# Kernel tuning notes

Measured on AMD Instinct MI355X. Metric: run time of the kernel, lower is better.

Reference implementation:

```python
import jax, jax.numpy as jnp
import numpy as np

E = 32      # num_experts
K = 4       # num_experts_per_tok
C = 1280


def setup_inputs() -> dict:
    key = jax.random.key(0)
    k0, k1, k2, k3, k4 = jax.random.split(key, 5)
    B, S, D, I = 4, 2048, 1024, 512
    return {
        "hidden_states": jax.random.normal(k0, (B, S, D), jnp.float32),
        "router_w": jax.random.normal(k1, (E, D), jnp.float32) * 0.02,   # nn.Linear(hidden, E).weight
        "gate_w": jax.random.normal(k2, (E, I, D), jnp.float32) * 0.02,
        "up_w": jax.random.normal(k3, (E, I, D), jnp.float32) * 0.02,
        "down_w": jax.random.normal(k4, (E, D, I), jnp.float32) * 0.02,
    }


def reference(hidden_states, router_w, gate_w, up_w, down_w):
    B, S, D = hidden_states.shape
    x = hidden_states.reshape(-1, D)                       # [T, D]
    T = x.shape[0]

    # Router: softmax in fp32, top-k, renormalize (norm_topk_prob=True)
    router_logits = x @ router_w.T                          # [T, E]
    probs = jax.nn.softmax(router_logits.astype(jnp.float32), axis=-1)
    w, sel = jax.lax.top_k(probs, K)                        # [T, K]
    w = w / jnp.sum(w, axis=-1, keepdims=True)
    w = w.astype(x.dtype)

    # Flatten (token, slot) dispatch rows
    e_flat = sel.reshape(-1)                                # [T*K]
    tok = jnp.repeat(jnp.arange(T), K)                      # [T*K]

    # Position of each row within its expert's buffer
    oh = jax.nn.one_hot(e_flat, E, dtype=jnp.int32)         # [T*K, E]
    pos = jnp.take_along_axis(jnp.cumsum(oh, axis=0), e_flat[:, None], axis=1)[:, 0] - 1
    valid = pos < C

    # Dispatch: scatter tokens into [E, C, D]; overflow rows go to slot C and are dropped
    pos_w = jnp.minimum(pos, C)
    buf = jnp.zeros((E, C + 1, D), x.dtype).at[e_flat, pos_w].set(x[tok])[:, :C]

    # Per-expert SwiGLU MLP as grouped matmuls
    g = jnp.einsum('ecd,eid->eci', buf, gate_w)
    u = jnp.einsum('ecd,eid->eci', buf, up_w)
    h = jax.nn.silu(g) * u
    y = jnp.einsum('eci,edi->ecd', h, down_w)               # [E, C, D]

    # Combine: gather expert outputs back and scatter-add into tokens
    pos_r = jnp.minimum(pos, C - 1)
    gathered = y[e_flat, pos_r]                             # [T*K, D]
    coef = w.reshape(-1) * valid.astype(x.dtype)
    final = jax.ops.segment_sum(gathered * coef[:, None], tok, num_segments=T)

    return final.reshape(B, S, D), router_logits
```

## Files before the change

### kernel.cpp

```cpp
#include <hip/hip_runtime.h>

#define T_TOK 8192
#define D_DIM 1024
#define E_NUM 32
#define K_TOP 4
#define CAP 1280
#define I_DIM 512

typedef float f32x4 __attribute__((ext_vector_type(4)));
typedef short s16x8 __attribute__((ext_vector_type(8)));

static __device__ __forceinline__ unsigned short f2bf(float f) {
    unsigned int u = __float_as_uint(f);
    unsigned int r = (u + 0x7fffu + ((u >> 16) & 1u)) >> 16;
    return (unsigned short)r;
}
static __device__ __forceinline__ float bf2f(unsigned short s) {
    return __uint_as_float(((unsigned int)s) << 16);
}

static __device__ __forceinline__ void gload16(const unsigned short* g, unsigned short* l) {
    __builtin_amdgcn_global_load_lds(
        (const __attribute__((address_space(1))) unsigned int*)g,
        (__attribute__((address_space(3))) unsigned int*)l,
        16, 0, 0);
}

#define GW_F4 4194304L
__global__ __launch_bounds__(256) void cvt_kernel(
    const float* __restrict__ gw,
    const float* __restrict__ uw, const float* __restrict__ dw,
    unsigned short* __restrict__ gbf,
    unsigned short* __restrict__ ubf, unsigned short* __restrict__ dbf) {
    long i = (long)blockIdx.x * 256 + threadIdx.x;
    const float* src; unsigned short* dst; long off;
    if (i < GW_F4)        { src = gw; dst = gbf; off = i; }
    else if (i < 2*GW_F4) { src = uw; dst = ubf; off = i - GW_F4; }
    else                  { src = dw; dst = dbf; off = i - 2*GW_F4; }
    float4 v = ((const float4*)src)[off];
    ushort4 b;
    b.x = f2bf(v.x); b.y = f2bf(v.y); b.z = f2bf(v.z); b.w = f2bf(v.w);
    ((ushort4*)dst)[off] = b;
}

__global__ __launch_bounds__(256) void router_kernel(
    const float* __restrict__ x, const float* __restrict__ rw,
    float* __restrict__ logits, unsigned short* __restrict__ xbf) {
    int t = (blockIdx.x * 256 + threadIdx.x) >> 6;
    int lane = threadIdx.x & 63;
    const float* xr = x + (size_t)t * D_DIM;
    float xf[16];
#pragma unroll
    for (int j = 0; j < 16; ++j) xf[j] = xr[lane + 64 * j];
    unsigned short* xb = xbf + (size_t)t * D_DIM;
#pragma unroll
    for (int j = 0; j < 16; ++j) xb[lane + 64 * j] = f2bf(xf[j]);
#pragma unroll 1
    for (int e = 0; e < E_NUM; ++e) {
        const float* wr = rw + (size_t)e * D_DIM;
        float acc = 0.f;
#pragma unroll
        for (int j = 0; j < 16; ++j) acc = fmaf(xf[j], wr[lane + 64 * j], acc);
#pragma unroll
        for (int off = 32; off; off >>= 1) acc += __shfl_xor(acc, off);
        if (lane == 0) logits[(size_t)t * E_NUM + e] = acc;
    }
}

__global__ __launch_bounds__(256) void topk_kernel(
    const float* __restrict__ logits,
    int* __restrict__ counts, int* __restrict__ rowtok,
    int* __restrict__ tokslot, float* __restrict__ tokcoef) {
    __shared__ float lg[256 * 33];
    __shared__ int hist[E_NUM];
    __shared__ int base[E_NUM];
    int tid = threadIdx.x;
    int t0 = blockIdx.x * 256;
    if (tid < E_NUM) hist[tid] = 0;
#pragma unroll
    for (int i = 0; i < E_NUM; ++i) {
        int idx = i * 256 + tid;
        lg[(idx >> 5) * 33 + (idx & 31)] = logits[(size_t)t0 * E_NUM + idx];
    }
    __syncthreads();

    float p[E_NUM];
    float m = -1e30f;
#pragma unroll
    for (int e = 0; e < E_NUM; ++e) { p[e] = lg[tid * 33 + e]; m = fmaxf(m, p[e]); }
#pragma unroll
    for (int e = 0; e < E_NUM; ++e) p[e] = __expf(p[e] - m);

    float wv[K_TOP]; int sel[K_TOP];
#pragma unroll
    for (int k = 0; k < K_TOP; ++k) {
        float best = -1.0f; int bi = 0;
#pragma unroll
        for (int e = 0; e < E_NUM; ++e) if (p[e] > best) { best = p[e]; bi = e; }
        wv[k] = best; sel[k] = bi; p[bi] = -2.0f;
    }

    int lofs[K_TOP];
#pragma unroll
    for (int k = 0; k < K_TOP; ++k) lofs[k] = atomicAdd(&hist[sel[k]], 1);
    __syncthreads();
    if (tid < E_NUM) base[tid] = atomicAdd(&counts[tid], hist[tid]);
    __syncthreads();

    float inv = 1.0f / (wv[0] + wv[1] + wv[2] + wv[3]);
    int t = t0 + tid;
#pragma unroll
    for (int k = 0; k < K_TOP; ++k) {
        int e = sel[k];
        int slot = base[e] + lofs[k];
        if (slot < CAP) {
            rowtok[e * CAP + slot] = t;
            tokslot[t * K_TOP + k] = e * CAP + slot;
        } else {
            tokslot[t * K_TOP + k] = -1;
        }
        tokcoef[t * K_TOP + k] = wv[k] * inv;
    }
}

__global__ __launch_bounds__(512, 2) void gateup_kernel(
    const unsigned short* __restrict__ xbf,
    const unsigned short* __restrict__ gbf, const unsigned short* __restrict__ ubf,
    const int* __restrict__ counts, const int* __restrict__ rowtok,
    unsigned short* __restrict__ h_ws) {
    int bid = blockIdx.x;
    int xcd = bid & 7;
    int slot = bid >> 3;
    int e = xcd + 8 * (slot / 20);
    int r = slot % 20;
    int mt = r >> 2;
    int nt = r & 3;
    int n_e = counts[e]; if (n_e > CAP) n_e = CAP;
    if (mt * 256 >= n_e) return;

    __shared__ unsigned short As[2][256 * 64];
    __shared__ unsigned short Bg[2][128 * 64];
    __shared__ unsigned short Bu[2][128 * 64];
    __shared__ int toks[256];

    int tid = threadIdx.x, lane = tid & 63, wv = tid >> 6;
    if (tid < 256) {
        int rr = mt * 256 + tid;
        toks[tid] = (rr < n_e) ? rowtok[e * CAP + rr] : rowtok[e * CAP];
    }
    __syncthreads();

    int row8 = tid >> 3;
    int c8 = (((tid & 7) ^ (row8 & 7)) * 8);
    int ldst = tid * 8;
    const unsigned short* aB[4];
#pragma unroll
    for (int j = 0; j < 4; ++j)
        aB[j] = xbf + (size_t)toks[j * 64 + row8] * D_DIM + c8;
    const unsigned short* gB[2];
    const unsigned short* uB[2];
#pragma unroll
    for (int j = 0; j < 2; ++j) {
        gB[j] = gbf + ((size_t)e * I_DIM + nt * 128 + j * 64 + row8) * D_DIM + c8;
        uB[j] = ubf + ((size_t)e * I_DIM + nt * 128 + j * 64 + row8) * D_DIM + c8;
    }

    int wm = (wv >> 1) * 64;
    int wn = (wv & 1) * 64;
    int fr = lane & 15;
    int fc = (lane >> 4) * 8;
    int fsw = (fr & 7) << 3;

    f32x4 accg[4][4] = {};
    f32x4 accu[4][4] = {};

    auto stage = [&](int kt) {
        int q = kt & 1, k2 = kt * 64;
#pragma unroll
        for (int j = 0; j < 4; ++j) gload16(aB[j] + k2, &As[q][j * 4096 + ldst]);
#pragma unroll
        for (int j = 0; j < 2; ++j) {
            gload16(gB[j] + k2, &Bg[q][j * 4096 + ldst]);
            gload16(uB[j] + k2, &Bu[q][j * 4096 + ldst]);
        }
    };
    auto compute = [&](int p) {
#pragma unroll
        for (int kk = 0; kk < 2; ++kk) {
            s16x8 af[4], bgf[4], buf_[4];
#pragma unroll
            for (int mi = 0; mi < 4; ++mi)
                af[mi] = *(const s16x8*)&As[p][(wm + mi * 16 + fr) * 64 + ((kk * 32 + fc) ^ fsw)];
#pragma unroll
            for (int ni = 0; ni < 4; ++ni) {
                bgf[ni]  = *(const s16x8*)&Bg[p][(wn + ni * 16 + fr) * 64 + ((kk * 32 + fc) ^ fsw)];
                buf_[ni] = *(const s16x8*)&Bu[p][(wn + ni * 16 + fr) * 64 + ((kk * 32 + fc) ^ fsw)];
            }
#pragma unroll
            for (int mi = 0; mi < 4; ++mi)
#pragma unroll
                for (int ni = 0; ni < 4; ++ni) {
                    accg[mi][ni] = __builtin_amdgcn_mfma_f32_16x16x32_bf16(af[mi], bgf[ni],  accg[mi][ni], 0, 0, 0);
                    accu[mi][ni] = __builtin_amdgcn_mfma_f32_16x16x32_bf16(af[mi], buf_[ni], accu[mi][ni], 0, 0, 0);
                }
        }
    };

    stage(0); stage(1);
    for (int kt = 0; kt < 15; ++kt) {
        int p = kt & 1;
        asm volatile("s_waitcnt vmcnt(8)" ::: "memory");
        asm volatile("s_barrier" ::: "memory");
        __builtin_amdgcn_s_setprio(1);
        compute(p);
        __builtin_amdgcn_s_setprio(0);
        asm volatile("s_barrier" ::: "memory");
        if (kt < 14) stage(kt + 2);
    }
    asm volatile("s_waitcnt vmcnt(0)" ::: "memory");
    asm volatile("s_barrier" ::: "memory");
    __builtin_amdgcn_s_setprio(1);
    compute(1);
    __builtin_amdgcn_s_setprio(0);

    int rq = (lane >> 4) * 4;
    int cq = lane & 15;
#pragma unroll
    for (int mi = 0; mi < 4; ++mi)
#pragma unroll
        for (int ni = 0; ni < 4; ++ni)
#pragma unroll
            for (int rr = 0; rr < 4; ++rr) {
                int grow = mt * 256 + wm + mi * 16 + rq + rr;
                if (grow < n_e) {
                    float g = accg[mi][ni][rr];
                    float hv = g / (1.0f + __expf(-g)) * accu[mi][ni][rr];
                    int icol = nt * 128 + wn + ni * 16 + cq;
                    h_ws[((size_t)e * CAP + grow) * I_DIM + icol] = f2bf(hv);
                }
            }
}

__global__ __launch_bounds__(512, 2) void down_kernel(
    const unsigned short* __restrict__ h_ws, const unsigned short* __restrict__ dbf,
    const int* __restrict__ counts, unsigned short* __restrict__ y_ws) {
    int bid = blockIdx.x;
    int xcd = bid & 7;
    int slot = bid >> 3;
    int e = xcd + 8 * (slot / 20);
    int r = slot % 20;
    int mt = r >> 2;
    int nt = r & 3;
    int n_e = counts[e]; if (n_e > CAP) n_e = CAP;
    if (mt * 256 >= n_e) return;

    __shared__ unsigned short As[2][256 * 64];
    __shared__ unsigned short Bd[2][256 * 64];

    int tid = threadIdx.x, lane = tid & 63, wv = tid >> 6;

    int row8 = tid >> 3;
    int c8 = (((tid & 7) ^ (row8 & 7)) * 8);
    int ldst = tid * 8;
    const unsigned short* aB[4];
    const unsigned short* bB[4];
#pragma unroll
    for (int j = 0; j < 4; ++j) {
        aB[j] = h_ws + ((size_t)e * CAP + mt * 256 + j * 64 + row8) * I_DIM + c8;
        bB[j] = dbf  + ((size_t)e * D_DIM + nt * 256 + j * 64 + row8) * I_DIM + c8;
    }

    int wm = (wv >> 2) * 128;
    int wn = (wv & 3) * 64;
    int fr = lane & 15;
    int fc = (lane >> 4) * 8;
    int fsw = (fr & 7) << 3;

    f32x4 acc[8][4] = {};

    auto stage = [&](int kt) {
        int q = kt & 1, k2 = kt * 64;
#pragma unroll
        for (int j = 0; j < 4; ++j) {
            gload16(aB[j] + k2, &As[q][j * 4096 + ldst]);
            gload16(bB[j] + k2, &Bd[q][j * 4096 + ldst]);
        }
    };
    auto compute = [&](int p) {
#pragma unroll
        for (int kk = 0; kk < 2; ++kk) {
            s16x8 af[8], bf[4];
#pragma unroll
            for (int mi = 0; mi < 8; ++mi)
                af[mi] = *(const s16x8*)&As[p][(wm + mi * 16 + fr) * 64 + ((kk * 32 + fc) ^ fsw)];
#pragma unroll
            for (int ni = 0; ni < 4; ++ni)
                bf[ni] = *(const s16x8*)&Bd[p][(wn + ni * 16 + fr) * 64 + ((kk * 32 + fc) ^ fsw)];
#pragma unroll
            for (int mi = 0; mi < 8; ++mi)
#pragma unroll
                for (int ni = 0; ni < 4; ++ni)
                    acc[mi][ni] = __builtin_amdgcn_mfma_f32_16x16x32_bf16(af[mi], bf[ni], acc[mi][ni], 0, 0, 0);
        }
    };

    stage(0); stage(1);
    for (int kt = 0; kt < 7; ++kt) {
        int p = kt & 1;
        asm volatile("s_waitcnt vmcnt(8)" ::: "memory");
        asm volatile("s_barrier" ::: "memory");
        __builtin_amdgcn_s_setprio(1);
        compute(p);
        __builtin_amdgcn_s_setprio(0);
        asm volatile("s_barrier" ::: "memory");
        if (kt < 6) stage(kt + 2);
    }
    asm volatile("s_waitcnt vmcnt(0)" ::: "memory");
    asm volatile("s_barrier" ::: "memory");
    __builtin_amdgcn_s_setprio(1);
    compute(1);
    __builtin_amdgcn_s_setprio(0);

    int rq = (lane >> 4) * 4;
    int cq = lane & 15;
#pragma unroll
    for (int mi = 0; mi < 8; ++mi)
#pragma unroll
        for (int ni = 0; ni < 4; ++ni)
#pragma unroll
            for (int rr = 0; rr < 4; ++rr) {
                int grow = mt * 256 + wm + mi * 16 + rq + rr;
                if (grow < n_e) {
                    int dcol = nt * 256 + wn + ni * 16 + cq;
                    y_ws[((size_t)e * CAP + grow) * D_DIM + dcol] = f2bf(acc[mi][ni][rr]);
                }
            }
}

__global__ __launch_bounds__(256) void combine_kernel(
    const unsigned short* __restrict__ y_ws,
    const int* __restrict__ tokslot, const float* __restrict__ tokcoef,
    float* __restrict__ out) {
    int t = (blockIdx.x * 256 + threadIdx.x) >> 6;
    int lane = threadIdx.x & 63;
    float acc[16] = {};
#pragma unroll
    for (int k = 0; k < K_TOP; ++k) {
        int slot = tokslot[t * K_TOP + k];
        if (slot >= 0) {
            float c = tokcoef[t * K_TOP + k];
            const unsigned short* row = y_ws + (size_t)slot * D_DIM + lane * 16;
            s16x8 v0 = *(const s16x8*)row;
            s16x8 v1 = *(const s16x8*)(row + 8);
#pragma unroll
            for (int j = 0; j < 8; ++j) acc[j]     = fmaf(c, bf2f((unsigned short)v0[j]), acc[j]);
#pragma unroll
            for (int j = 0; j < 8; ++j) acc[8 + j] = fmaf(c, bf2f((unsigned short)v1[j]), acc[8 + j]);
        }
    }
    float* o = out + (size_t)t * D_DIM + lane * 16;
#pragma unroll
    for (int j = 0; j < 4; ++j)
        ((float4*)o)[j] = make_float4(acc[4 * j], acc[4 * j + 1], acc[4 * j + 2], acc[4 * j + 3]);
}

extern "C" void kernel_launch(void* const* d_in, const int* in_sizes, int n_in,
                              void* d_out, int out_size, void* d_ws, size_t ws_size,
                              hipStream_t stream) {
    const float* x  = (const float*)d_in[0];
    const float* rw = (const float*)d_in[1];
    const float* gw = (const float*)d_in[2];
    const float* uw = (const float*)d_in[3];
    const float* dw = (const float*)d_in[4];
    float* out = (float*)d_out;
    float* logits = out + (size_t)T_TOK * D_DIM;

    char* ws = (char*)d_ws;
    size_t off = 0;
    unsigned short* xbf = (unsigned short*)(ws + off); off += (size_t)T_TOK * D_DIM * 2;
    unsigned short* gbf = (unsigned short*)(ws + off); off += (size_t)E_NUM * I_DIM * D_DIM * 2;
    unsigned short* ubf = (unsigned short*)(ws + off); off += (size_t)E_NUM * I_DIM * D_DIM * 2;
    unsigned short* y_ws = xbf;
    unsigned short* dbf = (unsigned short*)(ws + off); off += (size_t)E_NUM * D_DIM * I_DIM * 2;
    unsigned short* h_ws = (unsigned short*)(ws + off); off += (size_t)E_NUM * CAP * I_DIM * 2;
    int* counts = (int*)(ws + off); off += 256;
    int* rowtok = (int*)(ws + off); off += (size_t)E_NUM * CAP * 4;
    int* tokslot = (int*)(ws + off); off += (size_t)T_TOK * K_TOP * 4;
    float* tokcoef = (float*)(ws + off); off += (size_t)T_TOK * K_TOP * 4;

    hipMemsetAsync(counts, 0, E_NUM * 4, stream);

    cvt_kernel<<<(int)((3 * GW_F4) / 256), 256, 0, stream>>>(gw, uw, dw, gbf, ubf, dbf);
    router_kernel<<<T_TOK / 4, 256, 0, stream>>>(x, rw, logits, xbf);
    topk_kernel<<<T_TOK / 256, 256, 0, stream>>>(logits, counts, rowtok, tokslot, tokcoef);
    gateup_kernel<<<E_NUM * (CAP / 256) * (I_DIM / 128), 512, 0, stream>>>(xbf, gbf, ubf, counts, rowtok, h_ws);
    down_kernel<<<E_NUM * (CAP / 256) * (D_DIM / 256), 512, 0, stream>>>(h_ws, dbf, counts, y_ws);
    combine_kernel<<<T_TOK / 4, 256, 0, stream>>>(y_ws, tokslot, tokcoef, out);
}
```

Measured before the change: 465.1 us.

## Use 4-stage BK=32 LDS pipeline with single barrier per step in MoE GEMMs

Both the gate/up and down grouped GEMMs switch from a double-buffered 64-wide K tile to a four-deep ring of 32-wide K tiles. Each step issues the next loads right after one barrier, which drops the second barrier per iteration. It also changes the LDS swizzle for the narrower rows. The aim is to keep three tiles of loads in flight and cut synchronisation stalls. In exchange there are twice as many loop iterations and barriers per unit of K, and a new XOR pattern that may bring back bank conflicts.

```diff
diff --git a/kernel.cpp b/kernel.cpp
--- a/kernel.cpp
+++ b/kernel.cpp
@@ -138,9 +138,9 @@
     int n_e = counts[e]; if (n_e > CAP) n_e = CAP;
     if (mt * 256 >= n_e) return;
 
-    __shared__ unsigned short As[2][256 * 64];
-    __shared__ unsigned short Bg[2][128 * 64];
-    __shared__ unsigned short Bu[2][128 * 64];
+    __shared__ unsigned short As[4][256 * 32];
+    __shared__ unsigned short Bg[4][128 * 32];
+    __shared__ unsigned short Bu[4][128 * 32];
     __shared__ int toks[256];
 
     int tid = threadIdx.x, lane = tid & 63, wv = tid >> 6;
@@ -150,78 +150,58 @@
     }
     __syncthreads();
 
-    int row8 = tid >> 3;
-    int c8 = (((tid & 7) ^ (row8 & 7)) * 8);
+    int rA0 = tid >> 2;
+    int csw = ((tid & 3) ^ ((tid >> 3) & 3)) * 8;
+    const unsigned short* gaA0 = xbf + (size_t)toks[rA0] * D_DIM + csw;
+    const unsigned short* gaA1 = xbf + (size_t)toks[128 + rA0] * D_DIM + csw;
+    const unsigned short* gaG  = gbf + ((size_t)e * I_DIM + nt * 128 + rA0) * D_DIM + csw;
+    const unsigned short* gaU  = ubf + ((size_t)e * I_DIM + nt * 128 + rA0) * D_DIM + csw;
     int ldst = tid * 8;
-    const unsigned short* aB[4];
-#pragma unroll
-    for (int j = 0; j < 4; ++j)
-        aB[j] = xbf + (size_t)toks[j * 64 + row8] * D_DIM + c8;
-    const unsigned short* gB[2];
-    const unsigned short* uB[2];
-#pragma unroll
-    for (int j = 0; j < 2; ++j) {
-        gB[j] = gbf + ((size_t)e * I_DIM + nt * 128 + j * 64 + row8) * D_DIM + c8;
-        uB[j] = ubf + ((size_t)e * I_DIM + nt * 128 + j * 64 + row8) * D_DIM + c8;
-    }
 
     int wm = (wv >> 1) * 64;
     int wn = (wv & 1) * 64;
     int fr = lane & 15;
-    int fc = (lane >> 4) * 8;
-    int fsw = (fr & 7) << 3;
+    int pcol = (((lane >> 4) ^ ((fr >> 1) & 3)) * 8);
 
     f32x4 accg[4][4] = {};
     f32x4 accu[4][4] = {};
 
     auto stage = [&](int kt) {
-        int q = kt & 1, k2 = kt * 64;
-#pragma unroll
-        for (int j = 0; j < 4; ++j) gload16(aB[j] + k2, &As[q][j * 4096 + ldst]);
-#pragma unroll
-        for (int j = 0; j < 2; ++j) {
-            gload16(gB[j] + k2, &Bg[q][j * 4096 + ldst]);
-            gload16(uB[j] + k2, &Bu[q][j * 4096 + ldst]);
+        int b = kt & 3, k2 = kt * 32;
+        gload16(gaA0 + k2, &As[b][ldst]);
+        gload16(gaA1 + k2, &As[b][4096 + ldst]);
+        gload16(gaG  + k2, &Bg[b][ldst]);
+        gload16(gaU  + k2, &Bu[b][ldst]);
+    };
+
+    stage(0); stage(1); stage(2);
+    for (int kt = 0; kt < 32; ++kt) {
+        int b = kt & 3;
+        if (kt < 30)       asm volatile("s_waitcnt vmcnt(8)" ::: "memory");
+        else if (kt == 30) asm volatile("s_waitcnt vmcnt(4)" ::: "memory");
+        else               asm volatile("s_waitcnt vmcnt(0)" ::: "memory");
+        asm volatile("s_barrier" ::: "memory");
+        if (kt + 3 < 32) stage(kt + 3);
+
+        s16x8 af[4], bgf[4], buf_[4];
+#pragma unroll
+        for (int mi = 0; mi < 4; ++mi)
+            af[mi] = *(const s16x8*)&As[b][(wm + mi * 16 + fr) * 32 + pcol];
+#pragma unroll
+        for (int ni = 0; ni < 4; ++ni) {
+            bgf[ni]  = *(const s16x8*)&Bg[b][(wn + ni * 16 + fr) * 32 + pcol];
+            buf_[ni] = *(const s16x8*)&Bu[b][(wn + ni * 16 + fr) * 32 + pcol];
         }
-    };
-    auto compute = [&](int p) {
-#pragma unroll
-        for (int kk = 0; kk < 2; ++kk) {
-            s16x8 af[4], bgf[4], buf_[4];
-#pragma unroll
-            for (int mi = 0; mi < 4; ++mi)
-                af[mi] = *(const s16x8*)&As[p][(wm + mi * 16 + fr) * 64 + ((kk * 32 + fc) ^ fsw)];
+        __builtin_amdgcn_s_setprio(1);
+#pragma unroll
+        for (int mi = 0; mi < 4; ++mi)
 #pragma unroll
             for (int ni = 0; ni < 4; ++ni) {
-                bgf[ni]  = *(const s16x8*)&Bg[p][(wn + ni * 16 + fr) * 64 + ((kk * 32 + fc) ^ fsw)];
-                buf_[ni] = *(const s16x8*)&Bu[p][(wn + ni * 16 + fr) * 64 + ((kk * 32 + fc) ^ fsw)];
+                accg[mi][ni] = __builtin_amdgcn_mfma_f32_16x16x32_bf16(af[mi], bgf[ni],  accg[mi][ni], 0, 0, 0);
+                accu[mi][ni] = __builtin_amdgcn_mfma_f32_16x16x32_bf16(af[mi], buf_[ni], accu[mi][ni], 0, 0, 0);
             }
-#pragma unroll
-            for (int mi = 0; mi < 4; ++mi)
-#pragma unroll
-                for (int ni = 0; ni < 4; ++ni) {
-                    accg[mi][ni] = __builtin_amdgcn_mfma_f32_16x16x32_bf16(af[mi], bgf[ni],  accg[mi][ni], 0, 0, 0);
-                    accu[mi][ni] = __builtin_amdgcn_mfma_f32_16x16x32_bf16(af[mi], buf_[ni], accu[mi][ni], 0, 0, 0);
-                }
-        }
-    };
-
-    stage(0); stage(1);
-    for (int kt = 0; kt < 15; ++kt) {
-        int p = kt & 1;
-        asm volatile("s_waitcnt vmcnt(8)" ::: "memory");
-        asm volatile("s_barrier" ::: "memory");
-        __builtin_amdgcn_s_setprio(1);
-        compute(p);
         __builtin_amdgcn_s_setprio(0);
-        asm volatile("s_barrier" ::: "memory");
-        if (kt < 14) stage(kt + 2);
-    }
-    asm volatile("s_waitcnt vmcnt(0)" ::: "memory");
-    asm volatile("s_barrier" ::: "memory");
-    __builtin_amdgcn_s_setprio(1);
-    compute(1);
-    __builtin_amdgcn_s_setprio(0);
+    }
 
     int rq = (lane >> 4) * 4;
     int cq = lane & 15;
@@ -254,72 +234,58 @@
     int n_e = counts[e]; if (n_e > CAP) n_e = CAP;
     if (mt * 256 >= n_e) return;
 
-    __shared__ unsigned short As[2][256 * 64];
-    __shared__ unsigned short Bd[2][256 * 64];
+    __shared__ unsigned short As[4][256 * 32];
+    __shared__ unsigned short Bd[4][256 * 32];
 
     int tid = threadIdx.x, lane = tid & 63, wv = tid >> 6;
 
-    int row8 = tid >> 3;
-    int c8 = (((tid & 7) ^ (row8 & 7)) * 8);
+    int rA0 = tid >> 2;
+    int csw = ((tid & 3) ^ ((tid >> 3) & 3)) * 8;
+    const unsigned short* gaA0 = h_ws + ((size_t)e * CAP + mt * 256 + rA0) * I_DIM + csw;
+    const unsigned short* gaA1 = h_ws + ((size_t)e * CAP + mt * 256 + 128 + rA0) * I_DIM + csw;
+    const unsigned short* gaB0 = dbf  + ((size_t)e * D_DIM + nt * 256 + rA0) * I_DIM + csw;
+    const unsigned short* gaB1 = dbf  + ((size_t)e * D_DIM + nt * 256 + 128 + rA0) * I_DIM + csw;
     int ldst = tid * 8;
-    const unsigned short* aB[4];
-    const unsigned short* bB[4];
-#pragma unroll
-    for (int j = 0; j < 4; ++j) {
-        aB[j] = h_ws + ((size_t)e * CAP + mt * 256 + j * 64 + row8) * I_DIM + c8;
-        bB[j] = dbf  + ((size_t)e * D_DIM + nt * 256 + j * 64 + row8) * I_DIM + c8;
-    }
 
     int wm = (wv >> 2) * 128;
     int wn = (wv & 3) * 64;
     int fr = lane & 15;
-    int fc = (lane >> 4) * 8;
-    int fsw = (fr & 7) << 3;
+    int pcol = (((lane >> 4) ^ ((fr >> 1) & 3)) * 8);
 
     f32x4 acc[8][4] = {};
 
     auto stage = [&](int kt) {
-        int q = kt & 1, k2 = kt * 64;
-#pragma unroll
-        for (int j = 0; j < 4; ++j) {
-            gload16(aB[j] + k2, &As[q][j * 4096 + ldst]);
-            gload16(bB[j] + k2, &Bd[q][j * 4096 + ldst]);
-        }
+        int b = kt & 3, k2 = kt * 32;
+        gload16(gaA0 + k2, &As[b][ldst]);
+        gload16(gaA1 + k2, &As[b][4096 + ldst]);
+        gload16(gaB0 + k2, &Bd[b][ldst]);
+        gload16(gaB1 + k2, &Bd[b][4096 + ldst]);
     };
-    auto compute = [&](int p) {
-#pragma unroll
-        for (int kk = 0; kk < 2; ++kk) {
-            s16x8 af[8], bf[4];
-#pragma unroll
-            for (int mi = 0; mi < 8; ++mi)
-                af[mi] = *(const s16x8*)&As[p][(wm + mi * 16 + fr) * 64 + ((kk * 32 + fc) ^ fsw)];
+
+    stage(0); stage(1); stage(2);
+    for (int kt = 0; kt < 16; ++kt) {
+        int b = kt & 3;
+        if (kt < 14)       asm volatile("s_waitcnt vmcnt(8)" ::: "memory");
+        else if (kt == 14) asm volatile("s_waitcnt vmcnt(4)" ::: "memory");
+        else               asm volatile("s_waitcnt vmcnt(0)" ::: "memory");
+        asm volatile("s_barrier" ::: "memory");
+        if (kt + 3 < 16) stage(kt + 3);
+
+        s16x8 af[8], bf[4];
+#pragma unroll
+        for (int mi = 0; mi < 8; ++mi)
+            af[mi] = *(const s16x8*)&As[b][(wm + mi * 16 + fr) * 32 + pcol];
+#pragma unroll
+        for (int ni = 0; ni < 4; ++ni)
+            bf[ni] = *(const s16x8*)&Bd[b][(wn + ni * 16 + fr) * 32 + pcol];
+        __builtin_amdgcn_s_setprio(1);
+#pragma unroll
+        for (int mi = 0; mi < 8; ++mi)
 #pragma unroll
             for (int ni = 0; ni < 4; ++ni)
-                bf[ni] = *(const s16x8*)&Bd[p][(wn + ni * 16 + fr) * 64 + ((kk * 32 + fc) ^ fsw)];
-#pragma unroll
-            for (int mi = 0; mi < 8; ++mi)
-#pragma unroll
-                for (int ni = 0; ni < 4; ++ni)
-                    acc[mi][ni] = __builtin_amdgcn_mfma_f32_16x16x32_bf16(af[mi], bf[ni], acc[mi][ni], 0, 0, 0);
-        }
-    };
-
-    stage(0); stage(1);
-    for (int kt = 0; kt < 7; ++kt) {
-        int p = kt & 1;
-        asm volatile("s_waitcnt vmcnt(8)" ::: "memory");
-        asm volatile("s_barrier" ::: "memory");
-        __builtin_amdgcn_s_setprio(1);
-        compute(p);
+                acc[mi][ni] = __builtin_amdgcn_mfma_f32_16x16x32_bf16(af[mi], bf[ni], acc[mi][ni], 0, 0, 0);
         __builtin_amdgcn_s_setprio(0);
-        asm volatile("s_barrier" ::: "memory");
-        if (kt < 6) stage(kt + 2);
-    }
-    asm volatile("s_waitcnt vmcnt(0)" ::: "memory");
-    asm volatile("s_barrier" ::: "memory");
-    __builtin_amdgcn_s_setprio(1);
-    compute(1);
-    __builtin_amdgcn_s_setprio(0);
+    }
 
     int rq = (lane >> 4) * 4;
     int cq = lane & 15;
```

Measured after the change: 495.1 us. 6.5% more time.

## Make gate-up and down GEMMs loop over m-tiles with fixed grid

Applied to the files above, without the earlier changes.

Launches a fixed grid of 8 blocks per expert for both expert GEMM kernels; each block handles one n-tile and iterates over alternating m-tiles of its expert instead of one block per (m,n) tile. This is meant to remove the launch overhead of early-exit blocks for empty tiles and reuse weight tiles across m iterations. It risks lower occupancy (one block per CU) and serialized tiles lengthening the critical path.

```diff
diff --git a/kernel.cpp b/kernel.cpp
--- a/kernel.cpp
+++ b/kernel.cpp
@@ -129,14 +129,11 @@
     const int* __restrict__ counts, const int* __restrict__ rowtok,
     unsigned short* __restrict__ h_ws) {
     int bid = blockIdx.x;
-    int xcd = bid & 7;
-    int slot = bid >> 3;
-    int e = xcd + 8 * (slot / 20);
-    int r = slot % 20;
-    int mt = r >> 2;
-    int nt = r & 3;
+    int e = (bid & 7) + 8 * (bid >> 6);
+    int rem = (bid >> 3) & 7;
+    int nt = rem >> 1;
+    int h = rem & 1;
     int n_e = counts[e]; if (n_e > CAP) n_e = CAP;
-    if (mt * 256 >= n_e) return;
 
     __shared__ unsigned short As[2][256 * 64];
     __shared__ unsigned short Bg[2][128 * 64];
@@ -144,19 +141,10 @@
     __shared__ int toks[256];
 
     int tid = threadIdx.x, lane = tid & 63, wv = tid >> 6;
-    if (tid < 256) {
-        int rr = mt * 256 + tid;
-        toks[tid] = (rr < n_e) ? rowtok[e * CAP + rr] : rowtok[e * CAP];
-    }
-    __syncthreads();
 
     int row8 = tid >> 3;
     int c8 = (((tid & 7) ^ (row8 & 7)) * 8);
     int ldst = tid * 8;
-    const unsigned short* aB[4];
-#pragma unroll
-    for (int j = 0; j < 4; ++j)
-        aB[j] = xbf + (size_t)toks[j * 64 + row8] * D_DIM + c8;
     const unsigned short* gB[2];
     const unsigned short* uB[2];
 #pragma unroll
@@ -170,89 +158,100 @@
     int fr = lane & 15;
     int fc = (lane >> 4) * 8;
     int fsw = (fr & 7) << 3;
-
-    f32x4 accg[4][4] = {};
-    f32x4 accu[4][4] = {};
-
-    auto stage = [&](int kt) {
-        int q = kt & 1, k2 = kt * 64;
-#pragma unroll
-        for (int j = 0; j < 4; ++j) gload16(aB[j] + k2, &As[q][j * 4096 + ldst]);
-#pragma unroll
-        for (int j = 0; j < 2; ++j) {
-            gload16(gB[j] + k2, &Bg[q][j * 4096 + ldst]);
-            gload16(uB[j] + k2, &Bu[q][j * 4096 + ldst]);
+    int rq = (lane >> 4) * 4;
+    int cq = lane & 15;
+
+    for (int mt = h; mt < 5 && mt * 256 < n_e; mt += 2) {
+        __syncthreads();
+        if (tid < 256) {
+            int rr = mt * 256 + tid;
+            toks[tid] = (rr < n_e) ? rowtok[e * CAP + rr] : rowtok[e * CAP];
         }
-    };
-    auto compute = [&](int p) {
-#pragma unroll
-        for (int kk = 0; kk < 2; ++kk) {
-            s16x8 af[4], bgf[4], buf_[4];
-#pragma unroll
-            for (int mi = 0; mi < 4; ++mi)
-                af[mi] = *(const s16x8*)&As[p][(wm + mi * 16 + fr) * 64 + ((kk * 32 + fc) ^ fsw)];
-#pragma unroll
-            for (int ni = 0; ni < 4; ++ni) {
-                bgf[ni]  = *(const s16x8*)&Bg[p][(wn + ni * 16 + fr) * 64 + ((kk * 32 + fc) ^ fsw)];
-                buf_[ni] = *(const s16x8*)&Bu[p][(wn + ni * 16 + fr) * 64 + ((kk * 32 + fc) ^ fsw)];
+        __syncthreads();
+
+        const unsigned short* aB[4];
+#pragma unroll
+        for (int j = 0; j < 4; ++j)
+            aB[j] = xbf + (size_t)toks[j * 64 + row8] * D_DIM + c8;
+
+        f32x4 accg[4][4] = {};
+        f32x4 accu[4][4] = {};
+
+        auto stage = [&](int kt) {
+            int q = kt & 1, k2 = kt * 64;
+#pragma unroll
+            for (int j = 0; j < 4; ++j) gload16(aB[j] + k2, &As[q][j * 4096 + ldst]);
+#pragma unroll
+            for (int j = 0; j < 2; ++j) {
+                gload16(gB[j] + k2, &Bg[q][j * 4096 + ldst]);
+                gload16(uB[j] + k2, &Bu[q][j * 4096 + ldst]);
             }
-#pragma unroll
-            for (int mi = 0; mi < 4; ++mi)
+        };
+        auto compute = [&](int p) {
+#pragma unroll
+            for (int kk = 0; kk < 2; ++kk) {
+                s16x8 af[4], bgf[4], buf_[4];
+#pragma unroll
+                for (int mi = 0; mi < 4; ++mi)
+                    af[mi] = *(const s16x8*)&As[p][(wm + mi * 16 + fr) * 64 + ((kk * 32 + fc) ^ fsw)];
 #pragma unroll
                 for (int ni = 0; ni < 4; ++ni) {
-                    accg[mi][ni] = __builtin_amdgcn_mfma_f32_16x16x32_bf16(af[mi], bgf[ni],  accg[mi][ni], 0, 0, 0);
-                    accu[mi][ni] = __builtin_amdgcn_mfma_f32_16x16x32_bf16(af[mi], buf_[ni], accu[mi][ni], 0, 0, 0);
+                    bgf[ni]  = *(const s16x8*)&Bg[p][(wn + ni * 16 + fr) * 64 + ((kk * 32 + fc) ^ fsw)];
+                    buf_[ni] = *(const s16x8*)&Bu[p][(wn + ni * 16 + fr) * 64 + ((kk * 32 + fc) ^ fsw)];
                 }
+#pragma unroll
+                for (int mi = 0; mi < 4; ++mi)
+#pragma unroll
+                    for (int ni = 0; ni < 4; ++ni) {
+                        accg[mi][ni] = __builtin_amdgcn_mfma_f32_16x16x32_bf16(af[mi], bgf[ni],  accg[mi][ni], 0, 0, 0);
+                        accu[mi][ni] = __builtin_amdgcn_mfma_f32_16x16x32_bf16(af[mi], buf_[ni], accu[mi][ni], 0, 0, 0);
+                    }
+            }
+        };
+
+        stage(0); stage(1);
+        for (int kt = 0; kt < 15; ++kt) {
+            int p = kt & 1;
+            asm volatile("s_waitcnt vmcnt(8)" ::: "memory");
+            asm volatile("s_barrier" ::: "memory");
+            __builtin_amdgcn_s_setprio(1);
+            compute(p);
+            __builtin_amdgcn_s_setprio(0);
+            asm volatile("s_barrier" ::: "memory");
+            if (kt < 14) stage(kt + 2);
         }
-    };
-
-    stage(0); stage(1);
-    for (int kt = 0; kt < 15; ++kt) {
-        int p = kt & 1;
-        asm volatile("s_waitcnt vmcnt(8)" ::: "memory");
+        asm volatile("s_waitcnt vmcnt(0)" ::: "memory");
         asm volatile("s_barrier" ::: "memory");
         __builtin_amdgcn_s_setprio(1);
-        compute(p);
+        compute(1);
         __builtin_amdgcn_s_setprio(0);
-        asm volatile("s_barrier" ::: "memory");
-        if (kt < 14) stage(kt + 2);
-    }
-    asm volatile("s_waitcnt vmcnt(0)" ::: "memory");
-    asm volatile("s_barrier" ::: "memory");
-    __builtin_amdgcn_s_setprio(1);
-    compute(1);
-    __builtin_amdgcn_s_setprio(0);
-
-    int rq = (lane >> 4) * 4;
-    int cq = lane & 15;
-#pragma unroll
-    for (int mi = 0; mi < 4; ++mi)
-#pragma unroll
-        for (int ni = 0; ni < 4; ++ni)
-#pragma unroll
-            for (int rr = 0; rr < 4; ++rr) {
-                int grow = mt * 256 + wm + mi * 16 + rq + rr;
-                if (grow < n_e) {
-                    float g = accg[mi][ni][rr];
-                    float hv = g / (1.0f + __expf(-g)) * accu[mi][ni][rr];
-                    int icol = nt * 128 + wn + ni * 16 + cq;
-                    h_ws[((size_t)e * CAP + grow) * I_DIM + icol] = f2bf(hv);
+
+#pragma unroll
+        for (int mi = 0; mi < 4; ++mi)
+#pragma unroll
+            for (int ni = 0; ni < 4; ++ni)
+#pragma unroll
+                for (int rr = 0; rr < 4; ++rr) {
+                    int grow = mt * 256 + wm + mi * 16 + rq + rr;
+                    if (grow < n_e) {
+                        float g = accg[mi][ni][rr];
+                        float hv = g / (1.0f + __expf(-g)) * accu[mi][ni][rr];
+                        int icol = nt * 128 + wn + ni * 16 + cq;
+                        h_ws[((size_t)e * CAP + grow) * I_DIM + icol] = f2bf(hv);
+                    }
                 }
-            }
+    }
 }
 
 __global__ __launch_bounds__(512, 2) void down_kernel(
     const unsigned short* __restrict__ h_ws, const unsigned short* __restrict__ dbf,
     const int* __restrict__ counts, unsigned short* __restrict__ y_ws) {
     int bid = blockIdx.x;
-    int xcd = bid & 7;
-    int slot = bid >> 3;
-    int e = xcd + 8 * (slot / 20);
-    int r = slot % 20;
-    int mt = r >> 2;
-    int nt = r & 3;
+    int e = (bid & 7) + 8 * (bid >> 6);
+    int rem = (bid >> 3) & 7;
+    int nt = rem >> 1;
+    int h = rem & 1;
     int n_e = counts[e]; if (n_e > CAP) n_e = CAP;
-    if (mt * 256 >= n_e) return;
 
     __shared__ unsigned short As[2][256 * 64];
     __shared__ unsigned short Bd[2][256 * 64];
@@ -262,79 +261,85 @@
     int row8 = tid >> 3;
     int c8 = (((tid & 7) ^ (row8 & 7)) * 8);
     int ldst = tid * 8;
-    const unsigned short* aB[4];
     const unsigned short* bB[4];
 #pragma unroll
-    for (int j = 0; j < 4; ++j) {
-        aB[j] = h_ws + ((size_t)e * CAP + mt * 256 + j * 64 + row8) * I_DIM + c8;
-        bB[j] = dbf  + ((size_t)e * D_DIM + nt * 256 + j * 64 + row8) * I_DIM + c8;
-    }
+    for (int j = 0; j < 4; ++j)
+        bB[j] = dbf + ((size_t)e * D_DIM + nt * 256 + j * 64 + row8) * I_DIM + c8;
 
     int wm = (wv >> 2) * 128;
     int wn = (wv & 3) * 64;
     int fr = lane & 15;
     int fc = (lane >> 4) * 8;
     int fsw = (fr & 7) << 3;
-
-    f32x4 acc[8][4] = {};
-
-    auto stage = [&](int kt) {
-        int q = kt & 1, k2 = kt * 64;
-#pragma unroll
-        for (int j = 0; j < 4; ++j) {
-            gload16(aB[j] + k2, &As[q][j * 4096 + ldst]);
-            gload16(bB[j] + k2, &Bd[q][j * 4096 + ldst]);
+    int rq = (lane >> 4) * 4;
+    int cq = lane & 15;
+
+    for (int mt = h; mt < 5 && mt * 256 < n_e; mt += 2) {
+        __syncthreads();
+
+        const unsigned short* aB[4];
+#pragma unroll
+        for (int j = 0; j < 4; ++j)
+            aB[j] = h_ws + ((size_t)e * CAP + mt * 256 + j * 64 + row8) * I_DIM + c8;
+
+        f32x4 acc[8][4] = {};
+
+        auto stage = [&](int kt) {
+            int q = kt & 1, k2 = kt * 64;
+#pragma unroll
+            for (int j = 0; j < 4; ++j) {
+                gload16(aB[j] + k2, &As[q][j * 4096 + ldst]);
+                gload16(bB[j] + k2, &Bd[q][j * 4096 + ldst]);
+            }
+        };
+        auto compute = [&](int p) {
+#pragma unroll
+            for (int kk = 0; kk < 2; ++kk) {
+                s16x8 af[8], bf[4];
+#pragma unroll
+                for (int mi = 0; mi < 8; ++mi)
+                    af[mi] = *(const s16x8*)&As[p][(wm + mi * 16 + fr) * 64 + ((kk * 32 + fc) ^ fsw)];
+#pragma unroll
+                for (int ni = 0; ni < 4; ++ni)
+                    bf[ni] = *(const s16x8*)&Bd[p][(wn + ni * 16 + fr) * 64 + ((kk * 32 + fc) ^ fsw)];
+#pragma unroll
+                for (int mi = 0; mi < 8; ++mi)
+#pragma unroll
+                    for (int ni = 0; ni < 4; ++ni)
+                        acc[mi][ni] = __builtin_amdgcn_mfma_f32_16x16x32_bf16(af[mi], bf[ni], acc[mi][ni], 0, 0, 0);
+            }
+        };
+
+        stage(0); stage(1);
+        for (int kt = 0; kt < 7; ++kt) {
+            int p = kt & 1;
+            asm volatile("s_waitcnt vmcnt(8)" ::: "memory");
+            asm volatile("s_barrier" ::: "memory");
+            __builtin_amdgcn_s_setprio(1);
+            compute(p);
+            __builtin_amdgcn_s_setprio(0);
+            asm volatile("s_barrier" ::: "memory");
+            if (kt < 6) stage(kt + 2);
         }
-    };
-    auto compute = [&](int p) {
-#pragma unroll
-        for (int kk = 0; kk < 2; ++kk) {
-            s16x8 af[8], bf[4];
-#pragma unroll
-            for (int mi = 0; mi < 8; ++mi)
-                af[mi] = *(const s16x8*)&As[p][(wm + mi * 16 + fr) * 64 + ((kk * 32 + fc) ^ fsw)];
-#pragma unroll
-            for (int ni = 0; ni < 4; ++ni)
-                bf[ni] = *(const s16x8*)&Bd[p][(wn + ni * 16 + fr) * 64 + ((kk * 32 + fc) ^ fsw)];
-#pragma unroll
-            for (int mi = 0; mi < 8; ++mi)
-#pragma unroll
-                for (int ni = 0; ni < 4; ++ni)
-                    acc[mi][ni] = __builtin_amdgcn_mfma_f32_16x16x32_bf16(af[mi], bf[ni], acc[mi][ni], 0, 0, 0);
-        }
-    };
-
-    stage(0); stage(1);
-    for (int kt = 0; kt < 7; ++kt) {
-        int p = kt & 1;
-        asm volatile("s_waitcnt vmcnt(8)" ::: "memory");
+        asm volatile("s_waitcnt vmcnt(0)" ::: "memory");
         asm volatile("s_barrier" ::: "memory");
         __builtin_amdgcn_s_setprio(1);
-        compute(p);
+        compute(1);
         __builtin_amdgcn_s_setprio(0);
-        asm volatile("s_barrier" ::: "memory");
-        if (kt < 6) stage(kt + 2);
-    }
-    asm volatile("s_waitcnt vmcnt(0)" ::: "memory");
-    asm volatile("s_barrier" ::: "memory");
-    __builtin_amdgcn_s_setprio(1);
-    compute(1);
-    __builtin_amdgcn_s_setprio(0);
-
-    int rq = (lane >> 4) * 4;
-    int cq = lane & 15;
-#pragma unroll
-    for (int mi = 0; mi < 8; ++mi)
-#pragma unroll
-        for (int ni = 0; ni < 4; ++ni)
-#pragma unroll
-            for (int rr = 0; rr < 4; ++rr) {
-                int grow = mt * 256 + wm + mi * 16 + rq + rr;
-                if (grow < n_e) {
-                    int dcol = nt * 256 + wn + ni * 16 + cq;
-                    y_ws[((size_t)e * CAP + grow) * D_DIM + dcol] = f2bf(acc[mi][ni][rr]);
+
+#pragma unroll
+        for (int mi = 0; mi < 8; ++mi)
+#pragma unroll
+            for (int ni = 0; ni < 4; ++ni)
+#pragma unroll
+                for (int rr = 0; rr < 4; ++rr) {
+                    int grow = mt * 256 + wm + mi * 16 + rq + rr;
+                    if (grow < n_e) {
+                        int dcol = nt * 256 + wn + ni * 16 + cq;
+                        y_ws[((size_t)e * CAP + grow) * D_DIM + dcol] = f2bf(acc[mi][ni][rr]);
+                    }
                 }
-            }
+    }
 }
 
 __global__ __launch_bounds__(256) void combine_kernel(
@@ -393,7 +398,7 @@
     cvt_kernel<<<(int)((3 * GW_F4) / 256), 256, 0, stream>>>(gw, uw, dw, gbf, ubf, dbf);
     router_kernel<<<T_TOK / 4, 256, 0, stream>>>(x, rw, logits, xbf);
     topk_kernel<<<T_TOK / 256, 256, 0, stream>>>(logits, counts, rowtok, tokslot, tokcoef);
-    gateup_kernel<<<E_NUM * (CAP / 256) * (I_DIM / 128), 512, 0, stream>>>(xbf, gbf, ubf, counts, rowtok, h_ws);
-    down_kernel<<<E_NUM * (CAP / 256) * (D_DIM / 256), 512, 0, stream>>>(h_ws, dbf, counts, y_ws);
+    gateup_kernel<<<E_NUM * 8, 512, 0, stream>>>(xbf, gbf, ubf, counts, rowtok, h_ws);
+    down_kernel<<<E_NUM * 8, 512, 0, stream>>>(h_ws, dbf, counts, y_ws);
     combine_kernel<<<T_TOK / 4, 256, 0, stream>>>(y_ws, tokslot, tokcoef, out);
 }
```

After: 499.7 us. 7.4% more time.
